# Performance work log

Measured on AMD Instinct MI355X. Metric: run time of the kernel, lower is better.

The kernel has to match this reference:

```python
import jax, jax.numpy as jnp
import numpy as np

NY = NX = 256
NT = 256
B = 2
NSRC = 2
NREC = 64
DY = DX = 5.0
DT = 5e-4
PML = 20
PML_FREQ = 25.0


def setup_inputs() -> dict:
    key = jax.random.key(0)
    k1, k2, k3, k4, k5, k6 = jax.random.split(key, 6)
    # physically plausible elastic model
    vp = 3000.0 + 200.0 * jax.random.uniform(k1, (NY, NX), dtype=jnp.float32)
    vs = 1500.0 + 100.0 * jax.random.uniform(k2, (NY, NX), dtype=jnp.float32)
    rho = 2200.0 + 100.0 * jax.random.uniform(k3, (NY, NX), dtype=jnp.float32)
    lamb = rho * (vp ** 2 - 2.0 * vs ** 2)
    mu = rho * vs ** 2
    buoyancy = 1.0 / rho
    source_amplitudes_y = 1e3 * jax.random.normal(k4, (B, NSRC, NT), dtype=jnp.float32)
    lo, hi = PML + 10, NY - PML - 10  # keep sources/receivers inside the PML
    source_locations_y = jax.random.randint(k5, (B, NSRC, 2), lo, hi)
    receiver_locations_y = jax.random.randint(k6, (B, NREC, 2), lo, hi)
    return {
        "lamb": lamb,
        "mu": mu,
        "buoyancy": buoyancy,
        "source_amplitudes_y": source_amplitudes_y,
        "source_locations_y": source_locations_y,
        "receiver_locations_y": receiver_locations_y,
    }


def _pml_coeffs(n, width, dx, dt, max_vel, freq):
    # C-PML coefficients a, b along one axis; zero outside the PML region.
    i = jnp.arange(n, dtype=jnp.float32)
    frac = jnp.maximum(
        jnp.clip((width - i) / width, 0.0, 1.0),
        jnp.clip((i - (n - 1 - width)) / width, 0.0, 1.0),
    )
    sigma_max = 3.0 * max_vel * np.log(1000.0) / (2.0 * width * dx)
    sigma = sigma_max * frac ** 2
    alpha = np.pi * freq * (1.0 - frac)
    b = jnp.exp(-(sigma + alpha) * dt)
    a = sigma / (sigma + alpha + 1e-9) * (b - 1.0)
    return a, b


# staggered 2nd-order forward/backward differences (zero beyond the edge)
def _dfy(f):
    return jnp.pad(f[:, 1:] - f[:, :-1], ((0, 0), (0, 1), (0, 0))) / DY

def _dby(f):
    return jnp.pad(f[:, 1:] - f[:, :-1], ((0, 0), (1, 0), (0, 0))) / DY

def _dfx(f):
    return jnp.pad(f[:, :, 1:] - f[:, :, :-1], ((0, 0), (0, 0), (0, 1))) / DX

def _dbx(f):
    return jnp.pad(f[:, :, 1:] - f[:, :, :-1], ((0, 0), (0, 0), (1, 0))) / DX


def _forward(lamb, mu, buoyancy, amps, src_loc, rec_loc):
    ny, nx = lamb.shape
    bsz, nsrc, nt = amps.shape
    max_vel = jax.lax.stop_gradient(jnp.sqrt((lamb + 2.0 * mu) * buoyancy).max())
    ay, by = _pml_coeffs(ny, PML, DY, DT, max_vel, PML_FREQ)
    ax, bx = _pml_coeffs(nx, PML, DX, DT, max_vel, PML_FREQ)
    ay, by = ay[None, :, None], by[None, :, None]
    ax, bx = ax[None, None, :], bx[None, None, :]
    sb = jnp.arange(bsz)[:, None]
    sy, sx = src_loc[..., 0], src_loc[..., 1]
    ry, rx = rec_loc[..., 0], rec_loc[..., 1]
    src_scale = DT * buoyancy[sy, sx]  # [B, nsrc]
    l2m = lamb + 2.0 * mu
    z = jnp.zeros((bsz, ny, nx), lamb.dtype)
    fields0 = (z,) * 13  # vy, vx, syy, sxy, sxx + 8 PML memory fields

    def step(carry, amp_t):
        (vy, vx, syy, sxy, sxx,
         m_syyy, m_sxyx, m_sxyy, m_sxxx,
         m_vyy, m_vxx, m_vyx, m_vxy) = carry
        # velocity updates (with PML memory on stress derivatives)
        d = _dby(syy); m_syyy = by * m_syyy + ay * d; d_syy_y = d + m_syyy
        d = _dbx(sxy); m_sxyx = bx * m_sxyx + ax * d; d_sxy_x = d + m_sxyx
        vy = vy + DT * buoyancy * (d_syy_y + d_sxy_x)
        d = _dfy(sxy); m_sxyy = by * m_sxyy + ay * d; d_sxy_y = d + m_sxyy
        d = _dfx(sxx); m_sxxx = bx * m_sxxx + ax * d; d_sxx_x = d + m_sxxx
        vx = vx + DT * buoyancy * (d_sxy_y + d_sxx_x)
        # y-oriented source injection into vy
        vy = vy.at[sb, sy, sx].add(amp_t * src_scale)
        # stress updates (with PML memory on velocity derivatives)
        d = _dfy(vy); m_vyy = by * m_vyy + ay * d; d_vy_y = d + m_vyy
        d = _dbx(vx); m_vxx = bx * m_vxx + ax * d; d_vx_x = d + m_vxx
        syy = syy + DT * (l2m * d_vy_y + lamb * d_vx_x)
        sxx = sxx + DT * (lamb * d_vy_y + l2m * d_vx_x)
        d = _dbx(vy); m_vyx = bx * m_vyx + ax * d; d_vy_x = d + m_vyx
        d = _dby(vx); m_vxy = by * m_vxy + ay * d; d_vx_y = d + m_vxy
        sxy = sxy + DT * mu * (d_vy_x + d_vx_y)
        rec = vy[sb, ry, rx]  # [B, nrec]
        return (vy, vx, syy, sxy, sxx,
                m_syyy, m_sxyx, m_sxyy, m_sxxx,
                m_vyy, m_vxx, m_vyx, m_vxy), rec

    _, recs = jax.lax.scan(jax.checkpoint(step), fields0, jnp.transpose(amps, (2, 0, 1)))
    return jnp.transpose(recs, (1, 2, 0))  # [shot, receiver, time]


def reference(lamb, mu, buoyancy, source_amplitudes_y, source_locations_y, receiver_locations_y):
    return _forward(lamb, mu, buoyancy, source_amplitudes_y,
                    source_locations_y, receiver_locations_y)
```

## Files before the change

### kernel.cpp

```cpp
#include <hip/hip_runtime.h>

#define NYr 256
#define NXr 256
#define NTr 256
#define NBr 2
#define NSRCr 2
#define NRECr 64
#define NBLK 128
#define DTv 0.0005f
#define INVD 0.2f

#define COEF_OFF 0
#define TAG_F_OFF 1024
#define TBLK 2048

__device__ __forceinline__ unsigned long long tld(const unsigned long long* p) {
  return __hip_atomic_load(p, __ATOMIC_RELAXED, __HIP_MEMORY_SCOPE_AGENT);
}
__device__ __forceinline__ void tst(unsigned long long* p, float v, unsigned tag) {
  unsigned long long u = ((unsigned long long)tag << 32) | (unsigned long long)__float_as_uint(v);
  __hip_atomic_store(p, u, __ATOMIC_RELAXED, __HIP_MEMORY_SCOPE_AGENT);
}
#define TVAL(x) __uint_as_float((unsigned)(x))
#define TTAG(x) ((unsigned)((x) >> 32))

__device__ __forceinline__ void bar_lds() {
  asm volatile("s_waitcnt lgkmcnt(0)" ::: "memory");
  __builtin_amdgcn_s_barrier();
  asm volatile("" ::: "memory");
}

__global__ __launch_bounds__(256) void setup_kernel(
    const float* __restrict__ lamb, const float* __restrict__ mu,
    const float* __restrict__ buoy, float* __restrict__ coef)
{
  __shared__ float red[256];
  const int tid = threadIdx.x;
  float m = 0.0f;
  for (int i = tid; i < NYr*NXr; i += 256)
    m = fmaxf(m, sqrtf((lamb[i] + 2.0f*mu[i]) * buoy[i]));
  red[tid] = m;
  __syncthreads();
  for (int s = 128; s > 0; s >>= 1) {
    if (tid < s) red[tid] = fmaxf(red[tid], red[tid+s]);
    __syncthreads();
  }
  const float maxv = red[0];

  const float i_f = (float)tid;
  const float w = 20.0f;
  float f1 = fminf(fmaxf((w - i_f) * (1.0f/w), 0.0f), 1.0f);
  float f2 = fminf(fmaxf((i_f - (256.0f - 1.0f - w)) * (1.0f/w), 0.0f), 1.0f);
  float frac = fmaxf(f1, f2);
  float sigma_max = 3.0f * maxv * 6.907755278982137f / (2.0f * w * 5.0f);
  float sigma = sigma_max * frac * frac;
  float alpha = 3.14159265358979323f * 25.0f * (1.0f - frac);
  float bc = expf(-(sigma + alpha) * 0.0005f);
  float ac = sigma / (sigma + alpha + 1e-9f) * (bc - 1.0f);
  coef[tid]       = ac;
  coef[256 + tid] = bc;
  coef[512 + tid] = ac;
  coef[768 + tid] = bc;
}

__global__ __launch_bounds__(512) void elastic_tag3(
    const float* __restrict__ lamb_g, const float* __restrict__ mu_g,
    const float* __restrict__ buoy_g, const float* __restrict__ amps,
    const int* __restrict__ src_loc, const int* __restrict__ rec_loc,
    float* __restrict__ ws, float* __restrict__ out)
{
  __shared__ float S[3][4][NXr];
  __shared__ float V[2][6][NXr];

  const int blk = blockIdx.x;
  const int b = blk >> 6, bi = blk & 63;
  const int tid = threadIdx.x;
  const int ty = tid >> 8, tx = tid & 255;
  const int lo = bi << 2;
  const bool hasUp = bi > 0, hasDn = bi < 63;

  const float* coef = ws + COEF_OFF;
  unsigned long long* tagb = (unsigned long long*)(ws + TAG_F_OFF);

  const int txm = tx ? tx-1 : 0;
  const int txp = (tx < 255) ? tx+1 : 255;
  const bool xm_ok = tx > 0, xp_ok = tx < 255;
  const float axv = coef[512+tx], bxv = coef[768+tx];

  float vy_[3], vx_[3], myy[3], myx[3], mxyy[3], mxx[3];
  float dtb_[3], ayv[3], byv[3];
  #pragma unroll
  for (int k = 0; k < 3; ++k) {
    const int gy = lo - 1 + ty + 2*k;
    const bool ok = (gy >= 0) && (gy < NYr);
    const int gyc = ok ? gy : 0;
    dtb_[k] = ok ? DTv * buoy_g[gyc*NXr + tx] : 0.f;
    ayv[k]  = ok ? coef[gyc] : 0.f;
    byv[k]  = ok ? coef[256 + gyc] : 1.f;
    vy_[k] = vx_[k] = myy[k] = myx[k] = mxyy[k] = mxx[k] = 0.f;
  }
  float syy_[2], sxy_[2], sxx_[2], mvyy[2], mvxx[2], mvyx[2], mvxy[2];
  float lamv[2], muv[2], l2mv[2], ays[2], bys[2];
  #pragma unroll
  for (int j = 0; j < 2; ++j) {
    const int gy = lo + ty + 2*j;
    lamv[j] = lamb_g[gy*NXr + tx]; muv[j] = mu_g[gy*NXr + tx];
    l2mv[j] = lamv[j] + 2.f*muv[j];
    ays[j] = coef[gy]; bys[j] = coef[256 + gy];
    syy_[j] = sxy_[j] = sxx_[j] = 0.f;
    mvyy[j] = mvxx[j] = mvyx[j] = mvxy[j] = 0.f;
  }

  int sk0 = -1, sk1 = -1; int so0 = 0, so1 = 0;
  for (int i = 0; i < NBr*NSRCr; ++i) {
    const int sb = i >> 1, sy = src_loc[2*i], sx = src_loc[2*i+1];
    if (sb == b && sx == tx) {
      #pragma unroll
      for (int k = 0; k < 3; ++k) {
        const int gy = lo - 1 + ty + 2*k;
        if (gy == sy) { if (sk0 < 0) { sk0 = k; so0 = i*NTr; } else { sk1 = k; so1 = i*NTr; } }
      }
    }
  }
  const int gyA = ty ? lo     : lo + 1;
  const int gyB = ty ? lo + 2 : lo + 3;
  unsigned long long mA0=0, mA1=0, mB0=0, mB1=0;
  for (int i = 0; i < NBr*NRECr; ++i) {
    const int rb = i >> 6, ry = rec_loc[2*i], rx = rec_loc[2*i+1];
    if (rb == b && rx == tx) {
      if (ry == gyA) { if (i < 64) mA0 |= 1ull<<i; else mA1 |= 1ull<<(i-64); }
      if (ry == gyB) { if (i < 64) mB0 |= 1ull<<i; else mB1 |= 1ull<<(i-64); }
    }
  }
  const bool recA = (mA0|mA1) != 0ull, recB = (mB0|mB1) != 0ull;

  { float* p = &S[0][0][0]; for (int i = tid; i < 3*4*NXr; i += 512) p[i] = 0.f;
    float* q = &V[0][0][0]; for (int i = tid; i < 2*6*NXr; i += 512) q[i] = 0.f; }
  __syncthreads();

  for (int t = 0; t < NTr; ++t) {
    float a0 = 0.f, a1 = 0.f;
    if (sk0 >= 0) a0 = amps[so0 + t];
    if (sk1 >= 0) a1 = amps[so1 + t];

    unsigned long long u4w=0, u5w=0, u6w=0, u6mw=0, u7w=0, u7pw=0;
    unsigned long long d0w=0, d1w=0, d1mw=0, d2w=0, d3w=0, d3pw=0;
    const size_t pslot = (size_t)((t-1)&1)*NBLK;
    const unsigned long long* up = tagb + (pslot + (hasUp ? blk-1 : blk))*TBLK;
    const unsigned long long* dn = tagb + (pslot + (hasDn ? blk+1 : blk))*TBLK;
    if (t > 0) {
      if (ty == 0) {
        u4w = tld(up+4*256+tx); u5w = tld(up+5*256+tx); u6w = tld(up+6*256+tx);
        u6mw = tld(up+6*256+txm); u7w = tld(up+7*256+tx); u7pw = tld(up+7*256+txp);
        d1w = tld(dn+1*256+tx);
      } else {
        u5w = tld(up+5*256+tx);
        d0w = tld(dn+0*256+tx); d1w = tld(dn+1*256+tx); d1mw = tld(dn+1*256+txm);
        d2w = tld(dn+2*256+tx); d3w = tld(dn+3*256+tx); d3pw = tld(dn+3*256+txp);
      }
    }

    {
      const int sr = 1 + ty;
      float d, u1, u2, u3, u4;
      d = (S[0][sr][tx] - S[0][sr-1][tx]) * INVD;
      myy[1] = byv[1]*myy[1] + ayv[1]*d; u1 = d + myy[1];
      d = xm_ok ? (S[1][sr][tx] - S[1][sr][txm]) * INVD : 0.f;
      myx[1] = bxv*myx[1] + axv*d; u2 = d + myx[1];
      vy_[1] += dtb_[1]*(u1+u2);
      d = (S[1][sr+1][tx] - S[1][sr][tx]) * INVD;
      mxyy[1] = byv[1]*mxyy[1] + ayv[1]*d; u3 = d + mxyy[1];
      d = xp_ok ? (S[2][sr][txp] - S[2][sr][tx]) * INVD : 0.f;
      mxx[1] = bxv*mxx[1] + axv*d; u4 = d + mxx[1];
      vx_[1] += dtb_[1]*(u3+u4);
      if (sk0 == 1) vy_[1] += a0*dtb_[1];
      if (sk1 == 1) vy_[1] += a1*dtb_[1];
      V[0][ty+2][tx] = vy_[1];
      V[1][ty+2][tx] = vx_[1];
    }

    if (t > 0) {
      const unsigned want = (unsigned)t;
      if (ty == 0) {
        for (;;) {
          const bool okU = !hasUp || (TTAG(u4w)==want && TTAG(u5w)==want && TTAG(u6w)==want &&
                                      TTAG(u6mw)==want && TTAG(u7w)==want && TTAG(u7pw)==want);
          const bool okD = !hasDn || (TTAG(d1w)==want);
          if (okU && okD) break;
          u4w = tld(up+4*256+tx); u5w = tld(up+5*256+tx); u6w = tld(up+6*256+tx);
          u6mw = tld(up+6*256+txm); u7w = tld(up+7*256+tx); u7pw = tld(up+7*256+txp);
          d1w = tld(dn+1*256+tx);
        }
      } else {
        for (;;) {
          const bool okU = !hasUp || (TTAG(u5w)==want);
          const bool okD = !hasDn || (TTAG(d0w)==want && TTAG(d1w)==want && TTAG(d1mw)==want &&
                                      TTAG(d2w)==want && TTAG(d3w)==want && TTAG(d3pw)==want);
          if (okU && okD) break;
          u5w = tld(up+5*256+tx);
          d0w = tld(dn+0*256+tx); d1w = tld(dn+1*256+tx); d1mw = tld(dn+1*256+txm);
          d2w = tld(dn+2*256+tx); d3w = tld(dn+3*256+tx); d3pw = tld(dn+3*256+txp);
        }
      }
    }

    if (ty == 0) {
      if (hasUp) {
        const float syy2 = TVAL(u4w), syy3 = TVAL(u5w);
        const float sxy3t = TVAL(u6w), sxy3m = TVAL(u6mw);
        const float sxx3t = TVAL(u7w), sxx3p = TVAL(u7pw);
        float d, u1, u2, u3, u4;
        d = (syy3 - syy2) * INVD;
        myy[0] = byv[0]*myy[0] + ayv[0]*d; u1 = d + myy[0];
        d = xm_ok ? (sxy3t - sxy3m) * INVD : 0.f;
        myx[0] = bxv*myx[0] + axv*d; u2 = d + myx[0];
        vy_[0] += dtb_[0]*(u1+u2);
        d = (S[1][0][tx] - sxy3t) * INVD;
        mxyy[0] = byv[0]*mxyy[0] + ayv[0]*d; u3 = d + mxyy[0];
        d = xp_ok ? (sxx3p - sxx3t) * INVD : 0.f;
        mxx[0] = bxv*mxx[0] + axv*d; u4 = d + mxx[0];
        vx_[0] += dtb_[0]*(u3+u4);
        if (sk0 == 0) vy_[0] += a0*dtb_[0];
        if (sk1 == 0) vy_[0] += a1*dtb_[0];
        V[0][0][tx] = vy_[0]; V[1][0][tx] = vx_[0];
      }
      {
        const float sxy4t = TVAL(d1w);
        float d, u1, u2, u3, u4;
        d = (S[0][3][tx] - S[0][2][tx]) * INVD;
        myy[2] = byv[2]*myy[2] + ayv[2]*d; u1 = d + myy[2];
        d = xm_ok ? (S[1][3][tx] - S[1][3][txm]) * INVD : 0.f;
        myx[2] = bxv*myx[2] + axv*d; u2 = d + myx[2];
        vy_[2] += dtb_[2]*(u1+u2);
        d = hasDn ? (sxy4t - S[1][3][tx]) * INVD : 0.f;
        mxyy[2] = byv[2]*mxyy[2] + ayv[2]*d; u3 = d + mxyy[2];
        d = xp_ok ? (S[2][3][txp] - S[2][3][tx]) * INVD : 0.f;
        mxx[2] = bxv*mxx[2] + axv*d; u4 = d + mxx[2];
        vx_[2] += dtb_[2]*(u3+u4);
        if (sk0 == 2) vy_[2] += a0*dtb_[2];
        if (sk1 == 2) vy_[2] += a1*dtb_[2];
        V[0][4][tx] = vy_[2]; V[1][4][tx] = vx_[2];
      }
    } else {
      {
        const float syyU = TVAL(u5w);
        float d, u1, u2, u3, u4;
        d = hasUp ? (S[0][0][tx] - syyU) * INVD : 0.f;
        myy[0] = byv[0]*myy[0] + ayv[0]*d; u1 = d + myy[0];
        d = xm_ok ? (S[1][0][tx] - S[1][0][txm]) * INVD : 0.f;
        myx[0] = bxv*myx[0] + axv*d; u2 = d + myx[0];
        vy_[0] += dtb_[0]*(u1+u2);
        d = (S[1][1][tx] - S[1][0][tx]) * INVD;
        mxyy[0] = byv[0]*mxyy[0] + ayv[0]*d; u3 = d + mxyy[0];
        d = xp_ok ? (S[2][0][txp] - S[2][0][tx]) * INVD : 0.f;
        mxx[0] = bxv*mxx[0] + axv*d; u4 = d + mxx[0];
        vx_[0] += dtb_[0]*(u3+u4);
        if (sk0 == 0) vy_[0] += a0*dtb_[0];
        if (sk1 == 0) vy_[0] += a1*dtb_[0];
        V[0][1][tx] = vy_[0]; V[1][1][tx] = vx_[0];
      }
      if (hasDn) {
        const float syyD0 = TVAL(d0w), sxyD0t = TVAL(d1w), sxyD0m = TVAL(d1mw);
        const float sxyD1t = TVAL(d2w), sxxD0t = TVAL(d3w), sxxD0p = TVAL(d3pw);
        float d, u1, u2, u3, u4;
        d = (syyD0 - S[0][3][tx]) * INVD;
        myy[2] = byv[2]*myy[2] + ayv[2]*d; u1 = d + myy[2];
        d = xm_ok ? (sxyD0t - sxyD0m) * INVD : 0.f;
        myx[2] = bxv*myx[2] + axv*d; u2 = d + myx[2];
        vy_[2] += dtb_[2]*(u1+u2);
        d = (sxyD1t - sxyD0t) * INVD;
        mxyy[2] = byv[2]*mxyy[2] + ayv[2]*d; u3 = d + mxyy[2];
        d = xp_ok ? (sxxD0p - sxxD0t) * INVD : 0.f;
        mxx[2] = bxv*mxx[2] + axv*d; u4 = d + mxx[2];
        vx_[2] += dtb_[2]*(u3+u4);
        if (sk0 == 2) vy_[2] += a0*dtb_[2];
        if (sk1 == 2) vy_[2] += a1*dtb_[2];
        V[0][5][tx] = vy_[2]; V[1][5][tx] = vx_[2];
      }
    }

    bar_lds();

    unsigned long long* my = tagb + ((size_t)(t&1)*NBLK + blk)*TBLK;
    const unsigned wtag = (unsigned)(t + 1);
    #pragma unroll
    for (int j = 0; j < 2; ++j) {
      const int gy = lo + ty + 2*j;
      const int vr = ty + 2*j + 1;
      float d, u5, u6, u7, u8;
      d = (gy < NYr-1) ? (V[0][vr+1][tx] - V[0][vr][tx]) * INVD : 0.f;
      mvyy[j] = bys[j]*mvyy[j] + ays[j]*d; u5 = d + mvyy[j];
      d = xm_ok ? (V[1][vr][tx] - V[1][vr][txm]) * INVD : 0.f;
      mvxx[j] = bxv*mvxx[j] + axv*d; u6 = d + mvxx[j];
      syy_[j] += DTv*(l2mv[j]*u5 + lamv[j]*u6);
      sxx_[j] += DTv*(lamv[j]*u5 + l2mv[j]*u6);
      d = xm_ok ? (V[0][vr][tx] - V[0][vr][txm]) * INVD : 0.f;
      mvyx[j] = bxv*mvyx[j] + axv*d; u7 = d + mvyx[j];
      d = (gy > 0) ? (V[1][vr][tx] - V[1][vr-1][tx]) * INVD : 0.f;
      mvxy[j] = bys[j]*mvxy[j] + ays[j]*d; u8 = d + mvxy[j];
      sxy_[j] += DTv*muv[j]*(u7 + u8);
      const int r = ty + 2*j;
      if (r == 0) {
        tst(my + 0*256 + tx, syy_[j], wtag);
        tst(my + 1*256 + tx, sxy_[j], wtag);
        tst(my + 3*256 + tx, sxx_[j], wtag);
      } else if (r == 1) {
        tst(my + 2*256 + tx, sxy_[j], wtag);
      } else if (r == 2) {
        tst(my + 4*256 + tx, syy_[j], wtag);
      } else {
        tst(my + 5*256 + tx, syy_[j], wtag);
        tst(my + 6*256 + tx, sxy_[j], wtag);
        tst(my + 7*256 + tx, sxx_[j], wtag);
      }
      S[0][r][tx] = syy_[j]; S[1][r][tx] = sxy_[j]; S[2][r][tx] = sxx_[j];
    }
    bar_lds();

    if (recA) {
      const float v = ty ? vy_[0] : vy_[1];
      unsigned long long m = mA0; while (m) { int i = __ffsll((long long)m)-1; m &= m-1; out[i*NTr + t] = v; }
      m = mA1; while (m) { int i = __ffsll((long long)m)-1; m &= m-1; out[(i+64)*NTr + t] = v; }
    }
    if (recB) {
      const float v = ty ? vy_[1] : vy_[2];
      unsigned long long m = mB0; while (m) { int i = __ffsll((long long)m)-1; m &= m-1; out[i*NTr + t] = v; }
      m = mB1; while (m) { int i = __ffsll((long long)m)-1; m &= m-1; out[(i+64)*NTr + t] = v; }
    }
  }
}

extern "C" void kernel_launch(void* const* d_in, const int* in_sizes, int n_in,
                              void* d_out, int out_size, void* d_ws, size_t ws_size,
                              hipStream_t stream) {
  const float* lamb    = (const float*)d_in[0];
  const float* mu      = (const float*)d_in[1];
  const float* buoy    = (const float*)d_in[2];
  const float* amps    = (const float*)d_in[3];
  const int*   src_loc = (const int*)d_in[4];
  const int*   rec_loc = (const int*)d_in[5];
  float* out = (float*)d_out;
  float* ws  = (float*)d_ws;

  hipMemsetAsync((char*)ws + TAG_F_OFF*sizeof(float), 0,
                 (size_t)2*NBLK*TBLK*sizeof(unsigned long long), stream);

  hipLaunchKernelGGL(setup_kernel, dim3(1), dim3(256), 0, stream,
                     lamb, mu, buoy, ws + COEF_OFF);

  void* args[] = { (void*)&lamb, (void*)&mu, (void*)&buoy, (void*)&amps,
                   (void*)&src_loc, (void*)&rec_loc, (void*)&ws, (void*)&out };
  hipLaunchCooperativeKernel((void*)elastic_tag3, dim3(NBLK), dim3(512),
                             args, 0, stream);
}
```

Baseline: 667.0 us.

## Pack both shots into one 1024-thread workgroup per row slab

Instead of one 512-thread workgroup per (shot, 4-row slab), each workgroup now holds both shots for the same slab as two 512-thread halves with separate LDS buffers. The grid is halved to 64 workgroups and the tag exchange buffer is indexed by shot and node. The aim is to fill each CU better and halve the number of workgroups polling their neighbours, at the cost of larger workgroups and register pressure under 1024-thread launch bounds. The LDS barriers now cover both shots, so one shot can stall the other.

```diff
diff --git a/kernel.cpp b/kernel.cpp
--- a/kernel.cpp
+++ b/kernel.cpp
@@ -6,7 +6,7 @@
 #define NBr 2
 #define NSRCr 2
 #define NRECr 64
-#define NBLK 128
+#define NBLK 64
 #define DTv 0.0005f
 #define INVD 0.2f
 
@@ -63,21 +63,22 @@
   coef[768 + tid] = bc;
 }
 
-__global__ __launch_bounds__(512) void elastic_tag3(
+__global__ __launch_bounds__(1024) void elastic_2b(
     const float* __restrict__ lamb_g, const float* __restrict__ mu_g,
     const float* __restrict__ buoy_g, const float* __restrict__ amps,
     const int* __restrict__ src_loc, const int* __restrict__ rec_loc,
     float* __restrict__ ws, float* __restrict__ out)
 {
-  __shared__ float S[3][4][NXr];
-  __shared__ float V[2][6][NXr];
-
-  const int blk = blockIdx.x;
-  const int b = blk >> 6, bi = blk & 63;
+  __shared__ float S[2][3][4][NXr];
+  __shared__ float V[2][2][6][NXr];
+
+  const int node = blockIdx.x;
   const int tid = threadIdx.x;
-  const int ty = tid >> 8, tx = tid & 255;
-  const int lo = bi << 2;
-  const bool hasUp = bi > 0, hasDn = bi < 63;
+  const int b   = tid >> 9;
+  const int sub = tid & 511;
+  const int ty  = sub >> 8, tx = sub & 255;
+  const int lo = node << 2;
+  const bool hasUp = node > 0, hasDn = node < 63;
 
   const float* coef = ws + COEF_OFF;
   unsigned long long* tagb = (unsigned long long*)(ws + TAG_F_OFF);
@@ -134,8 +135,8 @@
   }
   const bool recA = (mA0|mA1) != 0ull, recB = (mB0|mB1) != 0ull;
 
-  { float* p = &S[0][0][0]; for (int i = tid; i < 3*4*NXr; i += 512) p[i] = 0.f;
-    float* q = &V[0][0][0]; for (int i = tid; i < 2*6*NXr; i += 512) q[i] = 0.f; }
+  { float* p = &S[0][0][0][0]; for (int i = tid; i < 2*3*4*NXr; i += 1024) p[i] = 0.f;
+    float* q = &V[0][0][0][0]; for (int i = tid; i < 2*2*6*NXr; i += 1024) q[i] = 0.f; }
   __syncthreads();
 
   for (int t = 0; t < NTr; ++t) {
@@ -145,9 +146,9 @@
 
     unsigned long long u4w=0, u5w=0, u6w=0, u6mw=0, u7w=0, u7pw=0;
     unsigned long long d0w=0, d1w=0, d1mw=0, d2w=0, d3w=0, d3pw=0;
-    const size_t pslot = (size_t)((t-1)&1)*NBLK;
-    const unsigned long long* up = tagb + (pslot + (hasUp ? blk-1 : blk))*TBLK;
-    const unsigned long long* dn = tagb + (pslot + (hasDn ? blk+1 : blk))*TBLK;
+    const size_t pbase = ((size_t)((t-1)&1)*2 + b)*NBLK;
+    const unsigned long long* up = tagb + (pbase + (hasUp ? node-1 : node))*TBLK;
+    const unsigned long long* dn = tagb + (pbase + (hasDn ? node+1 : node))*TBLK;
     if (t > 0) {
       if (ty == 0) {
         u4w = tld(up+4*256+tx); u5w = tld(up+5*256+tx); u6w = tld(up+6*256+tx);
@@ -163,20 +164,20 @@
     {
       const int sr = 1 + ty;
       float d, u1, u2, u3, u4;
-      d = (S[0][sr][tx] - S[0][sr-1][tx]) * INVD;
+      d = (S[b][0][sr][tx] - S[b][0][sr-1][tx]) * INVD;
       myy[1] = byv[1]*myy[1] + ayv[1]*d; u1 = d + myy[1];
-      d = xm_ok ? (S[1][sr][tx] - S[1][sr][txm]) * INVD : 0.f;
+      d = xm_ok ? (S[b][1][sr][tx] - S[b][1][sr][txm]) * INVD : 0.f;
       myx[1] = bxv*myx[1] + axv*d; u2 = d + myx[1];
       vy_[1] += dtb_[1]*(u1+u2);
-      d = (S[1][sr+1][tx] - S[1][sr][tx]) * INVD;
+      d = (S[b][1][sr+1][tx] - S[b][1][sr][tx]) * INVD;
       mxyy[1] = byv[1]*mxyy[1] + ayv[1]*d; u3 = d + mxyy[1];
-      d = xp_ok ? (S[2][sr][txp] - S[2][sr][tx]) * INVD : 0.f;
+      d = xp_ok ? (S[b][2][sr][txp] - S[b][2][sr][tx]) * INVD : 0.f;
       mxx[1] = bxv*mxx[1] + axv*d; u4 = d + mxx[1];
       vx_[1] += dtb_[1]*(u3+u4);
       if (sk0 == 1) vy_[1] += a0*dtb_[1];
       if (sk1 == 1) vy_[1] += a1*dtb_[1];
-      V[0][ty+2][tx] = vy_[1];
-      V[1][ty+2][tx] = vx_[1];
+      V[b][0][ty+2][tx] = vy_[1];
+      V[b][1][ty+2][tx] = vx_[1];
     }
 
     if (t > 0) {
@@ -215,55 +216,55 @@
         d = xm_ok ? (sxy3t - sxy3m) * INVD : 0.f;
         myx[0] = bxv*myx[0] + axv*d; u2 = d + myx[0];
         vy_[0] += dtb_[0]*(u1+u2);
-        d = (S[1][0][tx] - sxy3t) * INVD;
+        d = (S[b][1][0][tx] - sxy3t) * INVD;
         mxyy[0] = byv[0]*mxyy[0] + ayv[0]*d; u3 = d + mxyy[0];
         d = xp_ok ? (sxx3p - sxx3t) * INVD : 0.f;
         mxx[0] = bxv*mxx[0] + axv*d; u4 = d + mxx[0];
         vx_[0] += dtb_[0]*(u3+u4);
         if (sk0 == 0) vy_[0] += a0*dtb_[0];
         if (sk1 == 0) vy_[0] += a1*dtb_[0];
-        V[0][0][tx] = vy_[0]; V[1][0][tx] = vx_[0];
+        V[b][0][0][tx] = vy_[0]; V[b][1][0][tx] = vx_[0];
       }
       {
         const float sxy4t = TVAL(d1w);
         float d, u1, u2, u3, u4;
-        d = (S[0][3][tx] - S[0][2][tx]) * INVD;
+        d = (S[b][0][3][tx] - S[b][0][2][tx]) * INVD;
         myy[2] = byv[2]*myy[2] + ayv[2]*d; u1 = d + myy[2];
-        d = xm_ok ? (S[1][3][tx] - S[1][3][txm]) * INVD : 0.f;
+        d = xm_ok ? (S[b][1][3][tx] - S[b][1][3][txm]) * INVD : 0.f;
         myx[2] = bxv*myx[2] + axv*d; u2 = d + myx[2];
         vy_[2] += dtb_[2]*(u1+u2);
-        d = hasDn ? (sxy4t - S[1][3][tx]) * INVD : 0.f;
+        d = hasDn ? (sxy4t - S[b][1][3][tx]) * INVD : 0.f;
         mxyy[2] = byv[2]*mxyy[2] + ayv[2]*d; u3 = d + mxyy[2];
-        d = xp_ok ? (S[2][3][txp] - S[2][3][tx]) * INVD : 0.f;
+        d = xp_ok ? (S[b][2][3][txp] - S[b][2][3][tx]) * INVD : 0.f;
         mxx[2] = bxv*mxx[2] + axv*d; u4 = d + mxx[2];
         vx_[2] += dtb_[2]*(u3+u4);
         if (sk0 == 2) vy_[2] += a0*dtb_[2];
         if (sk1 == 2) vy_[2] += a1*dtb_[2];
-        V[0][4][tx] = vy_[2]; V[1][4][tx] = vx_[2];
+        V[b][0][4][tx] = vy_[2]; V[b][1][4][tx] = vx_[2];
       }
     } else {
       {
         const float syyU = TVAL(u5w);
         float d, u1, u2, u3, u4;
-        d = hasUp ? (S[0][0][tx] - syyU) * INVD : 0.f;
+        d = hasUp ? (S[b][0][0][tx] - syyU) * INVD : 0.f;
         myy[0] = byv[0]*myy[0] + ayv[0]*d; u1 = d + myy[0];
-        d = xm_ok ? (S[1][0][tx] - S[1][0][txm]) * INVD : 0.f;
+        d = xm_ok ? (S[b][1][0][tx] - S[b][1][0][txm]) * INVD : 0.f;
         myx[0] = bxv*myx[0] + axv*d; u2 = d + myx[0];
         vy_[0] += dtb_[0]*(u1+u2);
-        d = (S[1][1][tx] - S[1][0][tx]) * INVD;
+        d = (S[b][1][1][tx] - S[b][1][0][tx]) * INVD;
         mxyy[0] = byv[0]*mxyy[0] + ayv[0]*d; u3 = d + mxyy[0];
-        d = xp_ok ? (S[2][0][txp] - S[2][0][tx]) * INVD : 0.f;
+        d = xp_ok ? (S[b][2][0][txp] - S[b][2][0][tx]) * INVD : 0.f;
         mxx[0] = bxv*mxx[0] + axv*d; u4 = d + mxx[0];
         vx_[0] += dtb_[0]*(u3+u4);
         if (sk0 == 0) vy_[0] += a0*dtb_[0];
         if (sk1 == 0) vy_[0] += a1*dtb_[0];
-        V[0][1][tx] = vy_[0]; V[1][1][tx] = vx_[0];
+        V[b][0][1][tx] = vy_[0]; V[b][1][1][tx] = vx_[0];
       }
       if (hasDn) {
         const float syyD0 = TVAL(d0w), sxyD0t = TVAL(d1w), sxyD0m = TVAL(d1mw);
         const float sxyD1t = TVAL(d2w), sxxD0t = TVAL(d3w), sxxD0p = TVAL(d3pw);
         float d, u1, u2, u3, u4;
-        d = (syyD0 - S[0][3][tx]) * INVD;
+        d = (syyD0 - S[b][0][3][tx]) * INVD;
         myy[2] = byv[2]*myy[2] + ayv[2]*d; u1 = d + myy[2];
         d = xm_ok ? (sxyD0t - sxyD0m) * INVD : 0.f;
         myx[2] = bxv*myx[2] + axv*d; u2 = d + myx[2];
@@ -275,28 +276,28 @@
         vx_[2] += dtb_[2]*(u3+u4);
         if (sk0 == 2) vy_[2] += a0*dtb_[2];
         if (sk1 == 2) vy_[2] += a1*dtb_[2];
-        V[0][5][tx] = vy_[2]; V[1][5][tx] = vx_[2];
+        V[b][0][5][tx] = vy_[2]; V[b][1][5][tx] = vx_[2];
       }
     }
 
     bar_lds();
 
-    unsigned long long* my = tagb + ((size_t)(t&1)*NBLK + blk)*TBLK;
+    unsigned long long* my = tagb + (((size_t)(t&1)*2 + b)*NBLK + node)*TBLK;
     const unsigned wtag = (unsigned)(t + 1);
     #pragma unroll
     for (int j = 0; j < 2; ++j) {
       const int gy = lo + ty + 2*j;
       const int vr = ty + 2*j + 1;
       float d, u5, u6, u7, u8;
-      d = (gy < NYr-1) ? (V[0][vr+1][tx] - V[0][vr][tx]) * INVD : 0.f;
+      d = (gy < NYr-1) ? (V[b][0][vr+1][tx] - V[b][0][vr][tx]) * INVD : 0.f;
       mvyy[j] = bys[j]*mvyy[j] + ays[j]*d; u5 = d + mvyy[j];
-      d = xm_ok ? (V[1][vr][tx] - V[1][vr][txm]) * INVD : 0.f;
+      d = xm_ok ? (V[b][1][vr][tx] - V[b][1][vr][txm]) * INVD : 0.f;
       mvxx[j] = bxv*mvxx[j] + axv*d; u6 = d + mvxx[j];
       syy_[j] += DTv*(l2mv[j]*u5 + lamv[j]*u6);
       sxx_[j] += DTv*(lamv[j]*u5 + l2mv[j]*u6);
-      d = xm_ok ? (V[0][vr][tx] - V[0][vr][txm]) * INVD : 0.f;
+      d = xm_ok ? (V[b][0][vr][tx] - V[b][0][vr][txm]) * INVD : 0.f;
       mvyx[j] = bxv*mvyx[j] + axv*d; u7 = d + mvyx[j];
-      d = (gy > 0) ? (V[1][vr][tx] - V[1][vr-1][tx]) * INVD : 0.f;
+      d = (gy > 0) ? (V[b][1][vr][tx] - V[b][1][vr-1][tx]) * INVD : 0.f;
       mvxy[j] = bys[j]*mvxy[j] + ays[j]*d; u8 = d + mvxy[j];
       sxy_[j] += DTv*muv[j]*(u7 + u8);
       const int r = ty + 2*j;
@@ -313,7 +314,7 @@
         tst(my + 6*256 + tx, sxy_[j], wtag);
         tst(my + 7*256 + tx, sxx_[j], wtag);
       }
-      S[0][r][tx] = syy_[j]; S[1][r][tx] = sxy_[j]; S[2][r][tx] = sxx_[j];
+      S[b][0][r][tx] = syy_[j]; S[b][1][r][tx] = sxy_[j]; S[b][2][r][tx] = sxx_[j];
     }
     bar_lds();
 
@@ -343,13 +344,13 @@
   float* ws  = (float*)d_ws;
 
   hipMemsetAsync((char*)ws + TAG_F_OFF*sizeof(float), 0,
-                 (size_t)2*NBLK*TBLK*sizeof(unsigned long long), stream);
+                 (size_t)2*2*NBLK*TBLK*sizeof(unsigned long long), stream);
 
   hipLaunchKernelGGL(setup_kernel, dim3(1), dim3(256), 0, stream,
                      lamb, mu, buoy, ws + COEF_OFF);
 
   void* args[] = { (void*)&lamb, (void*)&mu, (void*)&buoy, (void*)&amps,
                    (void*)&src_loc, (void*)&rec_loc, (void*)&ws, (void*)&out };
-  hipLaunchCooperativeKernel((void*)elastic_tag3, dim3(NBLK), dim3(512),
+  hipLaunchCooperativeKernel((void*)elastic_2b, dim3(NBLK), dim3(1024),
                              args, 0, stream);
 }
```

Result: slower. 1.515 ms (+127.1%).
